# Kernel tuning notes

Hardware: AMD Instinct MI355X
Metric: run time of the kernel (lower is better)

Reference implementation:

```python
import jax, jax.numpy as jnp
import numpy as np

T, B, D = 512, 128, 1024  # time, batch, feature == hidden_size


def setup_inputs() -> dict:
    key = jax.random.key(0)
    k0, k1, k2, k3 = jax.random.split(key, 4)
    scale = 1.0 / np.sqrt(D)
    ins = jax.random.normal(k0, (T, B, D), jnp.float32)
    resets = jax.random.randint(k1, (T, B), 0, 2).astype(bool)
    # flax GRUCell params, fused along gate axis in order (r, z, n)
    Wi = jax.random.normal(k2, (D, 3 * D), jnp.float32) * scale   # ir|iz|in (with bias)
    bi = jnp.zeros((3 * D,), jnp.float32)
    Wh = jax.random.normal(k3, (D, 3 * D), jnp.float32) * scale   # hr|hz|hn (hr,hz no bias)
    bhn = jnp.zeros((D,), jnp.float32)                            # bias only on hn branch
    return {"ins": ins, "resets": resets, "Wi": Wi, "bi": bi, "Wh": Wh, "bhn": bhn}


def reference(ins, resets, Wi, bi, Wh, bhn):
    H = Wh.shape[0]
    # Input projections are time-independent: compute once as a big GEMM.
    xi = jnp.einsum('tbd,dg->tbg', ins, Wi) + bi  # [T, B, 3H]

    def step(h, inp):
        xi_t, reset_t = inp                       # [B, 3H], [B]
        h = jnp.where(reset_t[:, None], jnp.zeros_like(h), h)  # reset carry to zeros
        hh = h @ Wh                               # [B, 3H]
        xr, xz, xn = jnp.split(xi_t, 3, axis=-1)
        hr, hz, hn = jnp.split(hh, 3, axis=-1)
        r = jax.nn.sigmoid(xr + hr)
        z = jax.nn.sigmoid(xz + hz)
        n = jnp.tanh(xn + r * (hn + bhn))
        h_new = (1.0 - z) * n + z * h             # flax GRUCell update
        return h_new, h_new                       # GRUCell returns (new_h, new_h)

    h0 = jnp.zeros((ins.shape[1], H), ins.dtype)
    _, ys = jax.lax.scan(step, h0, (xi, resets))
    return ys  # [T, B, H]
```

## Files before the change

### kernel.cpp

```cpp
#include <hip/hip_runtime.h>
#include <stdint.h>

typedef unsigned short u16;
typedef unsigned int u32;
typedef unsigned char u8;

typedef __attribute__((ext_vector_type(4))) float f32x4;
typedef __attribute__((ext_vector_type(4))) u32 u32x4;
typedef __attribute__((ext_vector_type(8))) __bf16 bf16x8;

#define NITER 48
#define TT 512
#define BB 128

__device__ __forceinline__ u16 f2bf(float f){
    u32 u = __builtin_bit_cast(u32, f);
    u = (u + 0x7FFFu + ((u >> 16) & 1u)) >> 16;
    return (u16)u;
}
__device__ __forceinline__ float bf2f(u16 v){
    u32 u = ((u32)v) << 16;
    return __builtin_bit_cast(float, u);
}
__device__ __forceinline__ u32x4 pack8(f32x4 a, f32x4 b){
    u32x4 u;
    u[0] = (u32)f2bf(a[0]) | ((u32)f2bf(a[1]) << 16);
    u[1] = (u32)f2bf(a[2]) | ((u32)f2bf(a[3]) << 16);
    u[2] = (u32)f2bf(b[0]) | ((u32)f2bf(b[1]) << 16);
    u[3] = (u32)f2bf(b[2]) | ((u32)f2bf(b[3]) << 16);
    return u;
}
__device__ __forceinline__ void glds16(const u16* g, u16* l){
    __builtin_amdgcn_global_load_lds(
        (const __attribute__((address_space(1))) u32*)g,
        (__attribute__((address_space(3))) u32*)l, 16, 0, 0);
}

__global__ void k_detect(const u8* __restrict__ r, int* __restrict__ flag){
    __shared__ int nz[4];
    if (threadIdx.x < 4) nz[threadIdx.x] = 0;
    __syncthreads();
    int loc[4] = {0,0,0,0};
    const int base = threadIdx.x * 16;
    #pragma unroll
    for (int i = 0; i < 16; ++i) if (r[base + i]) loc[i & 3] = 1;
    #pragma unroll
    for (int j = 0; j < 4; ++j) if (loc[j]) atomicOr(&nz[j], 1);
    __syncthreads();
    if (threadIdx.x == 0){
        int f;
        if (nz[0] && !nz[1] && !nz[2] && !nz[3]) f = 0;
        else if (!nz[0] && !nz[1] && (nz[2] || nz[3])) f = 2;
        else f = 1;
        *flag = f;
    }
}

__device__ __forceinline__ int reset_at(const void* r, int f, int idx){
    if (f == 0) return ((const int*)r)[idx] != 0;
    if (f == 1) return ((const u8*)r)[idx] != 0;
    return ((const float*)r)[idx] != 0.f;
}

__global__ void k_ages(const void* __restrict__ resets, const int* __restrict__ flag,
                       int b0, int bw_log, u8* __restrict__ age, int* __restrict__ bh){
    __shared__ int lc[NITER];
    const int tid = threadIdx.x;
    if (tid < NITER) lc[tid] = 0;
    __syncthreads();
    const int cid = blockIdx.x * 256 + tid;
    const int f = *flag;
    const int bwm = (1 << bw_log) - 1;
    const int t = cid >> bw_log, b = b0 + (cid & bwm);
    int a = 0, tt = t;
    while (tt > 0 && !reset_at(resets, f, tt * BB + b)){ ++a; --tt; }
    if (a > NITER - 1) a = NITER - 1;
    age[cid] = (u8)a;
    atomicAdd(&lc[a], 1);
    __syncthreads();
    if (tid < NITER) bh[blockIdx.x * NITER + tid] = lc[tid];
}

__global__ void k_offsets(const int* __restrict__ bh, int NB,
                          int* __restrict__ counts, int* __restrict__ offs,
                          int* __restrict__ gbase, int* __restrict__ tbase,
                          int* __restrict__ bb){
    const int a = threadIdx.x;
    if (a < NITER){
        int run = 0;
        for (int b = 0; b < NB; ++b){
            bb[b * NITER + a] = run;
            run += bh[b * NITER + a];
        }
        counts[a] = run;
    }
    __syncthreads();
    if (a == 0){
        int o = 0;
        for (int i = 0; i < NITER; ++i){ offs[i] = o; o += counts[i]; }
        offs[NITER] = o;
        int g = 0, t = 0;
        for (int i = 0; i < NITER; ++i){
            const int ng = (counts[i] + 127) >> 7;
            gbase[i] = g; g += ng;
            tbase[i] = t; t += (i == 0) ? ng : ng * 16;
        }
        gbase[NITER] = g;
        tbase[NITER] = t;
    }
}

__global__ void k_scatter(const u8* __restrict__ age, const int* __restrict__ offs,
                          const int* __restrict__ bb,
                          u16* __restrict__ list, u16* __restrict__ posof){
    __shared__ u8 sa[256];
    const int tid = threadIdx.x;
    const int cid = blockIdx.x * 256 + tid;
    const int a = age[cid];
    sa[tid] = (u8)a;
    __syncthreads();
    int rank = 0;
    for (int j = 0; j < tid; ++j) rank += (sa[j] == (u8)a);
    const int pos = offs[a] + bb[blockIdx.x * NITER + a] + rank;
    list[pos] = (u16)cid;
    posof[cid] = (u16)pos;
}

__global__ void k_packT(const float* __restrict__ Wi, const float* __restrict__ Wh,
                        u16* __restrict__ Wit, u16* __restrict__ Wht){
    __shared__ float tl[32][33];
    const int kb = blockIdx.x * 32;
    const int nb = blockIdx.y * 32;
    const float* W = blockIdx.z ? Wh : Wi;
    u16* Wt = blockIdx.z ? Wht : Wit;
    const int tx = threadIdx.x;
    for (int r = threadIdx.y; r < 32; r += 8)
        tl[r][tx] = W[(size_t)(kb + r) * 3072 + nb + tx];
    __syncthreads();
    for (int r = threadIdx.y; r < 32; r += 8)
        Wt[(size_t)(nb + r) * 1024 + kb + tx] = f2bf(tl[tx][r]);
}

__global__ void k_tobf(const float* __restrict__ ins, u16* __restrict__ insbf,
                       int b0, int bw_log, int total8){
    const int bwm = (1 << bw_log) - 1;
    for (int i = blockIdx.x * 256 + threadIdx.x; i < total8; i += gridDim.x * 256){
        const int cid = i >> 7;
        const int c8 = (i & 127) * 8;
        const int t = cid >> bw_log, j = cid & bwm;
        const float* src = ins + (size_t)(t * BB + b0 + j) * 1024 + c8;
        f32x4 a = *(const f32x4*)src;
        f32x4 b = *(const f32x4*)(src + 4);
        *(u32x4*)(insbf + (size_t)cid * 1024 + c8) = pack8(a, b);
    }
}

__global__ __launch_bounds__(256, 4)
void k_xi(const u16* __restrict__ insbf, const u16* __restrict__ Wit,
          u16* __restrict__ xi, int Mrows)
{
    __shared__ __align__(16) u16 lds[2][8192];
    const int tid = threadIdx.x;
    const int lane = tid & 63;
    const int w = tid >> 6;
    const int wr = w >> 1, wc = w & 1;
    const int l15 = lane & 15;
    const int l4 = lane >> 4;

    const int nMt = Mrows >> 7;
    const int nTiles = nMt * 24;

    for (int idx = blockIdx.x; idx < nTiles; idx += gridDim.x){
        const int mt = idx / 24;
        const int cg = idx - mt * 24;
        const int m0 = mt * 128;
        const int c0 = cg * 128;

        const u16* ga0 = insbf + (size_t)(m0 + w * 16 + (lane >> 2)) * 1024 + (lane & 3) * 8;
        const u16* ga1 = ga0 + (size_t)64 * 1024;
        const u16* gb0 = Wit + (size_t)(c0 + w * 16 + (lane >> 2)) * 1024 + (lane & 3) * 8;
        const u16* gb1 = gb0 + (size_t)64 * 1024;

        f32x4 acc[4][4];
        #pragma unroll
        for (int i = 0; i < 4; ++i)
            #pragma unroll
            for (int j = 0; j < 4; ++j)
                acc[i][j] = (f32x4){0.f, 0.f, 0.f, 0.f};

        {
            u16* Lb = lds[0];
            glds16(ga0, &Lb[w * 512]);
            glds16(ga1, &Lb[2048 + w * 512]);
            glds16(gb0, &Lb[4096 + w * 512]);
            glds16(gb1, &Lb[6144 + w * 512]);
        }
        __syncthreads();

        for (int kt = 0; kt < 32; ++kt){
            if (kt < 31){
                u16* Nb = lds[(kt + 1) & 1];
                const int ko = (kt + 1) * 32;
                glds16(ga0 + ko, &Nb[w * 512]);
                glds16(ga1 + ko, &Nb[2048 + w * 512]);
                glds16(gb0 + ko, &Nb[4096 + w * 512]);
                glds16(gb1 + ko, &Nb[6144 + w * 512]);
            }
            const u16* L = lds[kt & 1];
            bf16x8 ax[4], bx[4];
            #pragma unroll
            for (int rf = 0; rf < 4; ++rf)
                ax[rf] = *(const bf16x8*)&L[(wr * 64 + rf * 16 + l15) * 32 + l4 * 8];
            #pragma unroll
            for (int cf = 0; cf < 4; ++cf)
                bx[cf] = *(const bf16x8*)&L[4096 + (wc * 64 + cf * 16 + l15) * 32 + l4 * 8];
            #pragma unroll
            for (int rf = 0; rf < 4; ++rf)
                #pragma unroll
                for (int cf = 0; cf < 4; ++cf)
                    acc[rf][cf] = __builtin_amdgcn_mfma_f32_16x16x32_bf16(
                        ax[rf], bx[cf], acc[rf][cf], 0, 0, 0);
            __syncthreads();
        }

        u16* region = ((u16*)lds) + w * 4096;
        #pragma unroll
        for (int rf = 0; rf < 4; ++rf)
            #pragma unroll
            for (int cf = 0; cf < 4; ++cf)
                #pragma unroll
                for (int m = 0; m < 4; ++m)
                    region[(rf * 16 + l4 * 4 + m) * 64 + cf * 16 + l15] = f2bf(acc[rf][cf][m]);
        #pragma unroll
        for (int rep = 0; rep < 8; ++rep){
            const int r = rep * 8 + (lane >> 3);
            const int cc = (lane & 7) * 8;
            u32x4 v = *(u32x4*)&region[r * 64 + cc];
            *(u32x4*)(xi + (size_t)(m0 + wr * 64 + r) * 3072 + c0 + wc * 64 + cc) = v;
        }
        __syncthreads();
    }
}

__device__ __forceinline__ void h0_body(int row, int c8, const u16* __restrict__ list,
    const u16* __restrict__ xi, float* __restrict__ ys, u16* __restrict__ hbf,
    const float* __restrict__ bi, const float* __restrict__ bhn, int b0, int bw_log)
{
    const int bwm = (1 << bw_log) - 1;
    const int cid = list[row];
    const int p = ((cid >> bw_log) << 7) + b0 + (cid & bwm);
    const u16* xr = xi + (size_t)cid * 3072 + c8;
    u32x4 vr = *(const u32x4*)xr;
    u32x4 vz = *(const u32x4*)(xr + 1024);
    u32x4 vn = *(const u32x4*)(xr + 2048);
    f32x4 br0 = *(const f32x4*)(bi + c8),        br1 = *(const f32x4*)(bi + c8 + 4);
    f32x4 bz0 = *(const f32x4*)(bi + 1024 + c8), bz1 = *(const f32x4*)(bi + 1024 + c8 + 4);
    f32x4 bn0 = *(const f32x4*)(bi + 2048 + c8), bn1 = *(const f32x4*)(bi + 2048 + c8 + 4);
    f32x4 bh0 = *(const f32x4*)(bhn + c8),       bh1 = *(const f32x4*)(bhn + c8 + 4);
    float out[8];
    #pragma unroll
    for (int e = 0; e < 8; ++e){
        const float xrv = bf2f((u16)(vr[e >> 1] >> ((e & 1) * 16)));
        const float xzv = bf2f((u16)(vz[e >> 1] >> ((e & 1) * 16)));
        const float xnv = bf2f((u16)(vn[e >> 1] >> ((e & 1) * 16)));
        const float brv = (e < 4) ? br0[e] : br1[e - 4];
        const float bzv = (e < 4) ? bz0[e] : bz1[e - 4];
        const float bnv = (e < 4) ? bn0[e] : bn1[e - 4];
        const float bhv = (e < 4) ? bh0[e] : bh1[e - 4];
        const float rr = 1.f / (1.f + __expf(-(xrv + brv)));
        const float zz = 1.f / (1.f + __expf(-(xzv + bzv)));
        const float nn = tanhf(xnv + bnv + rr * bhv);
        out[e] = (1.f - zz) * nn;
    }
    float* dst = ys + (size_t)p * 1024 + c8;
    f32x4 o0 = (f32x4){out[0], out[1], out[2], out[3]};
    f32x4 o1 = (f32x4){out[4], out[5], out[6], out[7]};
    *(f32x4*)dst = o0;
    *(f32x4*)(dst + 4) = o1;
    *(u32x4*)(hbf + (size_t)row * 1024 + c8) = pack8(o0, o1);
}

#define SSTR64 64
#define SAB 0
#define SBB 8192
#define SLB64 20480

__device__ __forceinline__ void scanh_tile(int mtg, int cg, int count, int off,
    int b0, int bw_log, const u16* __restrict__ list, const u16* __restrict__ posof,
    u16* hbf, const u16* __restrict__ xi, float* ys, const u16* __restrict__ Wht,
    const float* __restrict__ bi, const float* __restrict__ bhn,
    u16 (*lds)[SLB64])
{
    const int bwm = (1 << bw_log) - 1;
    const int bwv = 1 << bw_log;
    const int tid = threadIdx.x;
    const int lane = tid & 63;
    const int w = tid >> 6;
    const int wr = w >> 1;
    const int wc = w & 1;
    const int l15 = lane & 15;
    const int l4 = lane >> 4;
    const int lrow = lane >> 3;
    const int slot = lane & 7;

    const int m0 = mtg * 128;
    const int c0 = cg * 64;

    const u16* pa[4];
    #pragma unroll
    for (int c = 0; c < 4; ++c){
        const int r = c * 32 + w * 8 + lrow;
        const int cid = list[off + min(m0 + r, count - 1)];
        pa[c] = hbf + (size_t)posof[cid - bwv] * 1024 + slot * 8;
    }
    const u16* pw[6];
    #pragma unroll
    for (int c = 0; c < 6; ++c){
        const int br = c * 32 + w * 8 + lrow;
        const int g = br >> 6, ri = br & 63;
        pw[c] = Wht + (size_t)(g * 1024 + c0 + ri) * 1024 + slot * 8;
    }

    f32x4 acc[3][4][2];
    #pragma unroll
    for (int gi = 0; gi < 3; ++gi)
        #pragma unroll
        for (int rf = 0; rf < 4; ++rf)
            #pragma unroll
            for (int cf = 0; cf < 2; ++cf)
                acc[gi][rf][cf] = (f32x4){0.f, 0.f, 0.f, 0.f};

    {
        u16* N = lds[0];
        #pragma unroll
        for (int c = 0; c < 4; ++c)
            glds16(pa[c], &N[SAB + (c * 32 + w * 8) * SSTR64]);
        #pragma unroll
        for (int c = 0; c < 6; ++c)
            glds16(pw[c], &N[SBB + (c * 32 + w * 8) * SSTR64]);
    }
    __syncthreads();

    for (int kt = 0; kt < 16; ++kt){
        if (kt < 15){
            u16* N = lds[(kt + 1) & 1];
            const int ko = (kt + 1) * 64;
            #pragma unroll
            for (int c = 0; c < 4; ++c)
                glds16(pa[c] + ko, &N[SAB + (c * 32 + w * 8) * SSTR64]);
            #pragma unroll
            for (int c = 0; c < 6; ++c)
                glds16(pw[c] + ko, &N[SBB + (c * 32 + w * 8) * SSTR64]);
        }
        const u16* L = lds[kt & 1];
        #pragma unroll
        for (int kk = 0; kk < 2; ++kk){
            bf16x8 ah[4];
            #pragma unroll
            for (int rf = 0; rf < 4; ++rf)
                ah[rf] = *(const bf16x8*)&L[SAB + (wr * 64 + rf * 16 + l15) * SSTR64 + kk * 32 + l4 * 8];
            #pragma unroll
            for (int g = 0; g < 3; ++g){
                #pragma unroll
                for (int cf = 0; cf < 2; ++cf){
                    bf16x8 bh = *(const bf16x8*)&L[SBB + (g * 64 + wc * 32 + cf * 16 + l15) * SSTR64 + kk * 32 + l4 * 8];
                    #pragma unroll
                    for (int rf = 0; rf < 4; ++rf)
                        acc[g][rf][cf] = __builtin_amdgcn_mfma_f32_16x16x32_bf16(
                            ah[rf], bh, acc[g][rf][cf], 0, 0, 0);
                }
            }
        }
        __syncthreads();
    }

    #pragma unroll
    for (int cf = 0; cf < 2; ++cf){
        const int colh = c0 + wc * 32 + cf * 16 + l15;
        const float b_r = bi[colh];
        const float b_z = bi[1024 + colh];
        const float b_n = bi[2048 + colh];
        const float b_h = bhn[colh];
        #pragma unroll
        for (int rf = 0; rf < 4; ++rf){
            #pragma unroll
            for (int m = 0; m < 4; ++m){
                const int rloc = wr * 64 + rf * 16 + l4 * 4 + m;
                const int P = off + min(m0 + rloc, count - 1);
                const int cid = list[P];
                const int p = ((cid >> bw_log) << 7) + b0 + (cid & bwm);
                const u16* xr = xi + (size_t)cid * 3072 + colh;
                const float rr = 1.f / (1.f + __expf(-(bf2f(xr[0]) + b_r + acc[0][rf][cf][m])));
                const float zz = 1.f / (1.f + __expf(-(bf2f(xr[1024]) + b_z + acc[1][rf][cf][m])));
                const float nn = tanhf(bf2f(xr[2048]) + b_n + rr * (acc[2][rf][cf][m] + b_h));
                const float hp = ys[(size_t)(p - 128) * 1024 + colh];
                const float hv = (1.f - zz) * nn + zz * hp;
                ys[(size_t)p * 1024 + colh] = hv;
                hbf[(size_t)P * 1024 + colh] = f2bf(hv);
            }
        }
    }
}

__global__ __launch_bounds__(256, 2)
void k_scan_all(const u16* __restrict__ list, const int* __restrict__ offs,
                const int* __restrict__ counts, const u16* __restrict__ posof,
                u16* hbf, const u16* __restrict__ xi, float* ys,
                const u16* __restrict__ Wht, const float* __restrict__ bi,
                const float* __restrict__ bhn, int b0, int bw_log,
                const int* __restrict__ gbase, const int* __restrict__ tbase,
                u32* __restrict__ fin)
{
    __shared__ __align__(16) u16 lds[2][SLB64];
    const int T = tbase[NITER];
    const int tid = threadIdx.x;

    for (int idx = blockIdx.x; idx < T; idx += gridDim.x){
        int a = 0;
        while (tbase[a + 1] <= idx) ++a;

        if (a == 0){
            const int grp = idx;
            const int cnt0 = counts[0];
            const int nrows = min(128, cnt0 - grp * 128);
            for (int ii = tid; ii < nrows * 128; ii += 256){
                const int row = grp * 128 + (ii >> 7);
                const int c8 = (ii & 127) * 8;
                h0_body(row, c8, list, xi, ys, hbf, bi, bhn, b0, bw_log);
            }
            __syncthreads();
            if (tid == 0)
                __hip_atomic_fetch_add(&fin[gbase[0] + grp], 16u,
                                       __ATOMIC_RELEASE, __HIP_MEMORY_SCOPE_AGENT);
            continue;
        }

        const int rel = idx - tbase[a];
        const int mtg = rel >> 4, cg = rel & 15;
        const int count = counts[a], off = offs[a];

        if (tid == 0){
            const int bwv = 1 << bw_log;
            const int cidF = list[off + mtg * 128];
            const int cidL = list[off + min(mtg * 128 + 127, count - 1)];
            const int opv = offs[a - 1];
            const int glo = gbase[a - 1] + ((posof[cidF - bwv] - opv) >> 7);
            const int ghi = gbase[a - 1] + ((posof[cidL - bwv] - opv) >> 7);
            for (int g = glo; g <= ghi; ++g){
                while (__hip_atomic_load(&fin[g], __ATOMIC_RELAXED, __HIP_MEMORY_SCOPE_AGENT) < 16u)
                    __builtin_amdgcn_s_sleep(8);
            }
            (void)__hip_atomic_load(&fin[ghi], __ATOMIC_ACQUIRE, __HIP_MEMORY_SCOPE_AGENT);
        }
        __syncthreads();

        scanh_tile(mtg, cg, count, off, b0, bw_log, list, posof, hbf, xi, ys,
                   Wht, bi, bhn, lds);

        __syncthreads();
        if (tid == 0)
            __hip_atomic_fetch_add(&fin[gbase[a] + mtg], 1u,
                                   __ATOMIC_RELEASE, __HIP_MEMORY_SCOPE_AGENT);
    }
}

__global__ __launch_bounds__(256, 2)
void k_scan_fb(int iter, const u16* __restrict__ list, const int* __restrict__ offs,
               const int* __restrict__ counts, const float* __restrict__ ins,
               float* ys, const u16* __restrict__ Wit, const u16* __restrict__ Wht,
               const float* __restrict__ bi, const float* __restrict__ bhn)
{
    const int count = counts[iter];
    if (count <= 0) return;
    const int off = offs[iter];
    const int nTiles = ((count + 127) >> 7) * 16;
    const bool hasH = (iter > 0);

    __shared__ __align__(16) u16 lds[2][20480];

    const int tid = threadIdx.x;
    const int lane = tid & 63;
    const int w = tid >> 6;
    const int wr = w >> 1;
    const int wc = w & 1;
    const int l15 = lane & 15;
    const int l4 = lane >> 4;
    const int swz = ((l4 ^ (lane & 3)) * 8);
    const int sr = tid >> 2;
    const int sq = tid & 3;
    const int swzW = ((sq ^ (sr & 3)) * 8);

    for (int tile = blockIdx.x; tile < nTiles; tile += gridDim.x){
        const int mt = tile >> 4;
        const int cg = tile & 15;
        const int m0 = mt * 128;
        const int c0 = cg * 64;

        const int px0i = list[off + min(m0 + sr, count - 1)];
        const int px1i = list[off + min(m0 + 64 + sr, count - 1)];
        const float* px0 = ins + (size_t)px0i * 1024 + sq * 8;
        const float* px1 = ins + (size_t)px1i * 1024 + sq * 8;
        const float* ph0 = ys + (ptrdiff_t)(px0i - 128) * 1024 + sq * 8;
        const float* ph1 = ys + (ptrdiff_t)(px1i - 128) * 1024 + sq * 8;
        const u16* pb[6];
        #pragma unroll
        for (int pp = 0; pp < 6; ++pp){
            const int g = pp >> 1, m = pp & 1;
            const u16* W = m ? Wht : Wit;
            pb[pp] = W + (size_t)(g * 1024 + c0 + sr) * 1024 + sq * 8;
        }

        f32x4 acc[4][4][2];
        #pragma unroll
        for (int gi = 0; gi < 4; ++gi)
            #pragma unroll
            for (int rf = 0; rf < 4; ++rf)
                #pragma unroll
                for (int cf = 0; cf < 2; ++cf)
                    acc[gi][rf][cf] = (f32x4){0.f, 0.f, 0.f, 0.f};

        {
            u16* N = lds[0];
            *(u32x4*)&N[sr * 32 + swzW] = pack8(*(const f32x4*)(px0), *(const f32x4*)(px0 + 4));
            *(u32x4*)&N[(64 + sr) * 32 + swzW] = pack8(*(const f32x4*)(px1), *(const f32x4*)(px1 + 4));
            if (hasH){
                *(u32x4*)&N[(128 + sr) * 32 + swzW] = pack8(*(const f32x4*)(ph0), *(const f32x4*)(ph0 + 4));
                *(u32x4*)&N[(192 + sr) * 32 + swzW] = pack8(*(const f32x4*)(ph1), *(const f32x4*)(ph1 + 4));
            }
            #pragma unroll
            for (int pp = 0; pp < 6; ++pp)
                *(u32x4*)&N[8192 + (pp * 64 + sr) * 32 + swzW] = *(const u32x4*)(pb[pp]);
        }
        __syncthreads();

        int cur = 0;
        #pragma unroll 2
        for (int kt = 0; kt < 32; ++kt){
            f32x4 nx0a, nx0b, nx1a, nx1b, nh0a, nh0b, nh1a, nh1b;
            u32x4 sb[6];
            const bool more = (kt < 31);
            if (more){
                const int kof = (kt + 1) * 32;
                nx0a = *(const f32x4*)(px0 + kof); nx0b = *(const f32x4*)(px0 + kof + 4);
                nx1a = *(const f32x4*)(px1 + kof); nx1b = *(const f32x4*)(px1 + kof + 4);
                if (hasH){
                    nh0a = *(const f32x4*)(ph0 + kof); nh0b = *(const f32x4*)(ph0 + kof + 4);
                    nh1a = *(const f32x4*)(ph1 + kof); nh1b = *(const f32x4*)(ph1 + kof + 4);
                }
                #pragma unroll
                for (int pp = 0; pp < 6; ++pp) sb[pp] = *(const u32x4*)(pb[pp] + kof);
            }

            const u16* L = lds[cur];
            bf16x8 ax[4], ah[4];
            #pragma unroll
            for (int rf = 0; rf < 4; ++rf)
                ax[rf] = *(const bf16x8*)&L[(wr * 64 + rf * 16 + l15) * 32 + swz];
            if (hasH){
                #pragma unroll
                for (int rf = 0; rf < 4; ++rf)
                    ah[rf] = *(const bf16x8*)&L[(128 + wr * 64 + rf * 16 + l15) * 32 + swz];
            }
            #pragma unroll
            for (int g = 0; g < 3; ++g){
                #pragma unroll
                for (int cf = 0; cf < 2; ++cf){
                    const int brow = g * 128 + wc * 32 + cf * 16 + l15;
                    bf16x8 bv = *(const bf16x8*)&L[8192 + brow * 32 + swz];
                    const int gx = (g == 2) ? 2 : g;
                    #pragma unroll
                    for (int rf = 0; rf < 4; ++rf)
                        acc[gx][rf][cf] = __builtin_amdgcn_mfma_f32_16x16x32_bf16(
                            ax[rf], bv, acc[gx][rf][cf], 0, 0, 0);
                    if (hasH){
                        bf16x8 bh = *(const bf16x8*)&L[8192 + (brow + 64) * 32 + swz];
                        const int gh = (g == 2) ? 3 : g;
                        #pragma unroll
                        for (int rf = 0; rf < 4; ++rf)
                            acc[gh][rf][cf] = __builtin_amdgcn_mfma_f32_16x16x32_bf16(
                                ah[rf], bh, acc[gh][rf][cf], 0, 0, 0);
                    }
                }
            }

            if (more){
                u16* N = lds[cur ^ 1];
                *(u32x4*)&N[sr * 32 + swzW] = pack8(nx0a, nx0b);
                *(u32x4*)&N[(64 + sr) * 32 + swzW] = pack8(nx1a, nx1b);
                if (hasH){
                    *(u32x4*)&N[(128 + sr) * 32 + swzW] = pack8(nh0a, nh0b);
                    *(u32x4*)&N[(192 + sr) * 32 + swzW] = pack8(nh1a, nh1b);
                }
                #pragma unroll
                for (int pp = 0; pp < 6; ++pp)
                    *(u32x4*)&N[8192 + (pp * 64 + sr) * 32 + swzW] = sb[pp];
            }
            __syncthreads();
            cur ^= 1;
        }

        #pragma unroll
        for (int cf = 0; cf < 2; ++cf){
            const int colh = c0 + wc * 32 + cf * 16 + l15;
            const float b_r = bi[colh];
            const float b_z = bi[1024 + colh];
            const float b_n = bi[2048 + colh];
            const float b_h = bhn[colh];
            #pragma unroll
            for (int rf = 0; rf < 4; ++rf){
                #pragma unroll
                for (int m = 0; m < 4; ++m){
                    const int rloc = wr * 64 + rf * 16 + l4 * 4 + m;
                    const int p = list[off + min(m0 + rloc, count - 1)];
                    const float rr = 1.f / (1.f + __expf(-(acc[0][rf][cf][m] + b_r)));
                    const float zz = 1.f / (1.f + __expf(-(acc[1][rf][cf][m] + b_z)));
                    const float nn = tanhf(acc[2][rf][cf][m] + b_n + rr * (acc[3][rf][cf][m] + b_h));
                    float hp = 0.f;
                    if (hasH) hp = ys[(size_t)(p - 128) * 1024 + colh];
                    ys[(size_t)p * 1024 + colh] = (1.f - zz) * nn + zz * hp;
                }
            }
        }
    }
}

extern "C" void kernel_launch(void* const* d_in, const int* in_sizes, int n_in,
                              void* d_out, int out_size, void* d_ws, size_t ws_size,
                              hipStream_t stream)
{
    (void)in_sizes; (void)n_in; (void)out_size;
    const float* ins  = (const float*)d_in[0];
    const void*  rst  = d_in[1];
    const float* Wi   = (const float*)d_in[2];
    const float* bi   = (const float*)d_in[3];
    const float* Wh   = (const float*)d_in[4];
    const float* bhn  = (const float*)d_in[5];
    float* ys = (float*)d_out;
    u8* ws = (u8*)d_ws;

    const size_t A = 12648448;
    u16* Wit    = (u16*)(ws + 0);
    u16* Wht    = (u16*)(ws + 6291456);
    u8*  age    = ws + 12582912;
    int* counts = (int*)(ws + A + 0);
    int* offs   = (int*)(ws + A + 256);
    int* gbase  = (int*)(ws + A + 512);
    int* tbase  = (int*)(ws + A + 768);
    u32* fin    = (u32*)(ws + A + 1024);
    int* flag   = (int*)(ws + A + 5120);
    int* bh     = (int*)(ws + A + 5376);
    int* bb     = (int*)(ws + A + 54528);
    u16* posof  = (u16*)(ws + A + 103680);
    u16* list   = (u16*)(ws + A + 234752);
    u16* insbf  = (u16*)(ws + 13014272);

    int bw = 0, bwlog = 0;
    {
        const size_t base = 13014272;
        if (ws_size >= base + (size_t)TT * 128 * 8192)      { bw = 128; bwlog = 7; }
        else if (ws_size >= base + (size_t)TT * 64 * 8192)  { bw = 64;  bwlog = 6; }
        else if (ws_size >= base + (size_t)TT * 32 * 8192)  { bw = 32;  bwlog = 5; }
    }

    k_detect<<<1, 256, 0, stream>>>((const u8*)rst, flag);
    k_packT<<<dim3(32, 96, 2), dim3(32, 8), 0, stream>>>(Wi, Wh, Wit, Wht);

    if (bw == 0){
        const int Mr = TT * BB, NB = Mr / 256;
        hipMemsetAsync(ws + A, 0, 5120, stream);
        k_ages<<<NB, 256, 0, stream>>>(rst, flag, 0, 7, age, bh);
        k_offsets<<<1, 64, 0, stream>>>(bh, NB, counts, offs, gbase, tbase, bb);
        k_scatter<<<NB, 256, 0, stream>>>(age, offs, bb, list, posof);
        for (int it = 0; it < NITER; ++it)
            k_scan_fb<<<512, 256, 0, stream>>>(it, list, offs, counts, ins, ys, Wit, Wht, bi, bhn);
        return;
    }

    u16* xi = insbf + (size_t)TT * bw * 1024;
    u16* hbf = insbf;
    const int nch = BB / bw;
    const int Mrows = TT * bw;
    const int NB = Mrows / 256;

    for (int c = 0; c < nch; ++c){
        const int b0 = c * bw;
        hipMemsetAsync(ws + A, 0, 5120, stream);
        k_ages<<<NB, 256, 0, stream>>>(rst, flag, b0, bwlog, age, bh);
        k_offsets<<<1, 64, 0, stream>>>(bh, NB, counts, offs, gbase, tbase, bb);
        k_scatter<<<NB, 256, 0, stream>>>(age, offs, bb, list, posof);
        k_tobf<<<2048, 256, 0, stream>>>(ins, insbf, b0, bwlog, Mrows * 128);
        k_xi<<<3072, 256, 0, stream>>>(insbf, Wit, xi, Mrows);
        k_scan_all<<<512, 256, 0, stream>>>(list, offs, counts, posof, hbf, xi, ys,
                                            Wht, bi, bhn, b0, bwlog, gbase, tbase, fin);
    }
}
```

Baseline: 2.136 ms.

## Run early large scan iterations as separate launches, persistent kernel for tail

The age-0 init and the first few age levels, which have many rows, are pulled out of the persistent k_scan_all kernel. They now run as a dedicated k_h0 launch followed by per-iteration k_scanh launches with grid sizes derived from an estimated row count. Launch boundaries replace the atomic flag spin-waits for these levels, and the persistent kernel starts at ASTART with no dependency wait at its first level. The trade-off is more kernel launches and the loss of overlap between the early levels, in exchange for removing spin-wait and polling overhead where the work is widest.

```diff
diff --git a/kernel.cpp b/kernel.cpp
--- a/kernel.cpp
+++ b/kernel.cpp
@@ -12,6 +12,7 @@
 #define NITER 48
 #define TT 512
 #define BB 128
+#define ASTART 6
 
 __device__ __forceinline__ u16 f2bf(float f){
     u32 u = __builtin_bit_cast(u32, f);
@@ -280,6 +281,16 @@
     *(u32x4*)(hbf + (size_t)row * 1024 + c8) = pack8(o0, o1);
 }
 
+__global__ void k_h0(const u16* __restrict__ list, const int* __restrict__ counts,
+                     const u16* __restrict__ xi, float* __restrict__ ys,
+                     u16* __restrict__ hbf, const float* __restrict__ bi,
+                     const float* __restrict__ bhn, int b0, int bw_log)
+{
+    const int total = counts[0] * 128;
+    for (int i = blockIdx.x * 256 + threadIdx.x; i < total; i += gridDim.x * 256)
+        h0_body(i >> 7, (i & 127) * 8, list, xi, ys, hbf, bi, bhn, b0, bw_log);
+}
+
 #define SSTR64 64
 #define SAB 0
 #define SBB 8192
@@ -403,56 +414,61 @@
 }
 
 __global__ __launch_bounds__(256, 2)
+void k_scanh(int iter, const u16* __restrict__ list, const int* __restrict__ offs,
+             const int* __restrict__ counts, const u16* __restrict__ posof,
+             u16* hbf, const u16* __restrict__ xi,
+             float* ys, const u16* __restrict__ Wht,
+             const float* __restrict__ bi, const float* __restrict__ bhn,
+             int b0, int bw_log)
+{
+    const int count = counts[iter];
+    if (count <= 0) return;
+    const int off = offs[iter];
+    const int nTiles = ((count + 127) >> 7) * 16;
+    __shared__ __align__(16) u16 lds[2][SLB64];
+    for (int tile = blockIdx.x; tile < nTiles; tile += gridDim.x)
+        scanh_tile(tile >> 4, tile & 15, count, off, b0, bw_log, list, posof,
+                   hbf, xi, ys, Wht, bi, bhn, lds);
+}
+
+__global__ __launch_bounds__(256, 2)
 void k_scan_all(const u16* __restrict__ list, const int* __restrict__ offs,
                 const int* __restrict__ counts, const u16* __restrict__ posof,
                 u16* hbf, const u16* __restrict__ xi, float* ys,
                 const u16* __restrict__ Wht, const float* __restrict__ bi,
                 const float* __restrict__ bhn, int b0, int bw_log,
                 const int* __restrict__ gbase, const int* __restrict__ tbase,
-                u32* __restrict__ fin)
+                u32* __restrict__ fin, int aStart)
 {
     __shared__ __align__(16) u16 lds[2][SLB64];
     const int T = tbase[NITER];
     const int tid = threadIdx.x;
 
-    for (int idx = blockIdx.x; idx < T; idx += gridDim.x){
-        int a = 0;
+    for (int idx = tbase[aStart] + blockIdx.x; idx < T; idx += gridDim.x){
+        int a = aStart;
         while (tbase[a + 1] <= idx) ++a;
-
-        if (a == 0){
-            const int grp = idx;
-            const int cnt0 = counts[0];
-            const int nrows = min(128, cnt0 - grp * 128);
-            for (int ii = tid; ii < nrows * 128; ii += 256){
-                const int row = grp * 128 + (ii >> 7);
-                const int c8 = (ii & 127) * 8;
-                h0_body(row, c8, list, xi, ys, hbf, bi, bhn, b0, bw_log);
-            }
-            __syncthreads();
-            if (tid == 0)
-                __hip_atomic_fetch_add(&fin[gbase[0] + grp], 16u,
-                                       __ATOMIC_RELEASE, __HIP_MEMORY_SCOPE_AGENT);
-            continue;
-        }
 
         const int rel = idx - tbase[a];
         const int mtg = rel >> 4, cg = rel & 15;
         const int count = counts[a], off = offs[a];
-
-        if (tid == 0){
-            const int bwv = 1 << bw_log;
-            const int cidF = list[off + mtg * 128];
-            const int cidL = list[off + min(mtg * 128 + 127, count - 1)];
-            const int opv = offs[a - 1];
-            const int glo = gbase[a - 1] + ((posof[cidF - bwv] - opv) >> 7);
-            const int ghi = gbase[a - 1] + ((posof[cidL - bwv] - opv) >> 7);
-            for (int g = glo; g <= ghi; ++g){
-                while (__hip_atomic_load(&fin[g], __ATOMIC_RELAXED, __HIP_MEMORY_SCOPE_AGENT) < 16u)
-                    __builtin_amdgcn_s_sleep(8);
-            }
-            (void)__hip_atomic_load(&fin[ghi], __ATOMIC_ACQUIRE, __HIP_MEMORY_SCOPE_AGENT);
-        }
-        __syncthreads();
+        if (count <= 0) continue;
+
+        if (a > aStart){
+            if (tid == 0){
+                const int bwv = 1 << bw_log;
+                const int cidF = list[off + min(mtg * 128, count - 1)];
+                const int cidL = list[off + min(mtg * 128 + 127, count - 1)];
+                const int opv = offs[a - 1];
+                const int glo = gbase[a - 1] + ((posof[cidF - bwv] - opv) >> 7);
+                const int ghi = gbase[a - 1] + ((posof[cidL - bwv] - opv) >> 7);
+                for (int g = glo; g <= ghi; ++g){
+                    while (__hip_atomic_load(&fin[g], __ATOMIC_RELAXED, __HIP_MEMORY_SCOPE_AGENT) < 16u)
+                        __builtin_amdgcn_s_sleep(8);
+                }
+                (void)__hip_atomic_load(&fin[ghi], __ATOMIC_ACQUIRE, __HIP_MEMORY_SCOPE_AGENT);
+            }
+            __syncthreads();
+        }
 
         scanh_tile(mtg, cg, count, off, b0, bw_log, list, posof, hbf, xi, ys,
                    Wht, bi, bhn, lds);
@@ -690,7 +706,15 @@
         k_scatter<<<NB, 256, 0, stream>>>(age, offs, bb, list, posof);
         k_tobf<<<2048, 256, 0, stream>>>(ins, insbf, b0, bwlog, Mrows * 128);
         k_xi<<<3072, 256, 0, stream>>>(insbf, Wit, xi, Mrows);
+        k_h0<<<2048, 256, 0, stream>>>(list, counts, xi, ys, hbf, bi, bhn, b0, bwlog);
+        for (int it = 1; it < ASTART; ++it){
+            int est = ((Mrows >> (it + 1)) / 128 + 1) * 16;
+            int grid = est < 32 ? 32 : (est > 512 ? 512 : est);
+            k_scanh<<<grid, 256, 0, stream>>>(it, list, offs, counts, posof, hbf, xi,
+                                              ys, Wht, bi, bhn, b0, bwlog);
+        }
         k_scan_all<<<512, 256, 0, stream>>>(list, offs, counts, posof, hbf, xi, ys,
-                                            Wht, bi, bhn, b0, bwlog, gbase, tbase, fin);
-    }
-}
+                                            Wht, bi, bhn, b0, bwlog, gbase, tbase,
+                                            fin, ASTART);
+    }
+}
```

New measurement: 1.820 ms. 14.8% less time.
